# Kernel optimization log

Hardware: AMD Instinct MI355X
Metric: run time of the kernel (lower is better)

## Reference

```python
import jax, jax.numpy as jnp
import numpy as np

S, V, E, H = 4096, 10000, 128, 256
NE, TK, NH, HD, FF, NL = 4, 2, 4, 64, 2048, 2
EPS = 1e-5
SCALE = 1.0 / np.sqrt(HD).astype(np.float32)


def setup_inputs() -> dict:
    key = jax.random.key(0)
    ks = iter(jax.random.split(key, 64))
    n = lambda shape: jax.random.normal(next(ks), shape, jnp.float32) * 0.02
    inp = {"x": jax.random.randint(next(ks), (S,), 0, V)}
    inp["emb"] = n((V, E))
    for i, din in enumerate([E, H, H]):
        inp[f"moe{i}_gw"] = n((NE, din))
        inp[f"moe{i}_gb"] = jnp.zeros((NE,), jnp.float32)
        inp[f"moe{i}_ew"] = n((NE, H, din))
        inp[f"moe{i}_eb"] = jnp.zeros((NE, H), jnp.float32)
    inp["attn_in_w"] = n((NL, 3 * H, H)); inp["attn_in_b"] = jnp.zeros((NL, 3 * H), jnp.float32)
    inp["attn_out_w"] = n((NL, H, H));    inp["attn_out_b"] = jnp.zeros((NL, H), jnp.float32)
    inp["ln1_g"] = jnp.ones((NL, H), jnp.float32); inp["ln1_b"] = jnp.zeros((NL, H), jnp.float32)
    inp["ln2_g"] = jnp.ones((NL, H), jnp.float32); inp["ln2_b"] = jnp.zeros((NL, H), jnp.float32)
    inp["ff1_w"] = n((NL, FF, H)); inp["ff1_b"] = jnp.zeros((NL, FF), jnp.float32)
    inp["ff2_w"] = n((NL, H, FF)); inp["ff2_b"] = jnp.zeros((NL, H), jnp.float32)
    inp["fc_w"] = n((H, H)); inp["fc_b"] = jnp.zeros((H,), jnp.float32)
    inp["out_w"] = n((V, H)); inp["out_b"] = jnp.zeros((V,), jnp.float32)
    return inp


def _ln(x, g, b):
    m = x.mean(-1, keepdims=True)
    v = ((x - m) ** 2).mean(-1, keepdims=True)
    return (x - m) * jax.lax.rsqrt(v + EPS) * g + b


def _moe(x, gw, gb, ew, eb):
    # x: [S, din]. Faithful quirk: experts are the top-k of TOKEN 0's gates,
    # applied to every token, weighted by each token's own top-k gate scores.
    scores = jax.nn.softmax(x @ gw.T + gb, axis=-1)            # [S, NE]
    vals, idx = jax.lax.top_k(scores, TK)                      # [S, TK]
    sel = idx[0]                                               # [TK]
    outs = jnp.einsum('si,khi->skh', x, ew[sel]) + eb[sel][None]  # [S, TK, H]
    return (outs * vals[:, :, None]).sum(axis=1)               # [S, H]


def reference(x, emb,
              moe0_gw, moe0_gb, moe0_ew, moe0_eb,
              moe1_gw, moe1_gb, moe1_ew, moe1_eb,
              moe2_gw, moe2_gb, moe2_ew, moe2_eb,
              attn_in_w, attn_in_b, attn_out_w, attn_out_b,
              ln1_g, ln1_b, ln2_g, ln2_b,
              ff1_w, ff1_b, ff2_w, ff2_b,
              fc_w, fc_b, out_w, out_b):
    h = emb[x]                                                 # [S, E]
    for gw, gb, ew, eb in [(moe0_gw, moe0_gb, moe0_ew, moe0_eb),
                           (moe1_gw, moe1_gb, moe1_ew, moe1_eb),
                           (moe2_gw, moe2_gb, moe2_ew, moe2_eb)]:
        h = _moe(h, gw, gb, ew, eb)                            # [S, H]
    for l in range(NL):  # post-norm TransformerEncoderLayer (relu, no dropout at eval)
        qkv = h @ attn_in_w[l].T + attn_in_b[l]                # [S, 3H]
        q, k, v = [t.reshape(S, NH, HD) for t in jnp.split(qkv, 3, axis=-1)]
        att = jax.nn.softmax(jnp.einsum('shd,thd->hst', q, k) * SCALE, axis=-1)
        a = jnp.einsum('hst,thd->shd', att, v).reshape(S, H)
        h = _ln(h + a @ attn_out_w[l].T + attn_out_b[l], ln1_g[l], ln1_b[l])
        ffh = jax.nn.relu(h @ ff1_w[l].T + ff1_b[l]) @ ff2_w[l].T + ff2_b[l]
        h = _ln(h + ffh, ln2_g[l], ln2_b[l])
    h = h @ fc_w.T + fc_b                                      # [S, H]
    logits = h @ out_w.T + out_b                               # [S, V]
    return jax.nn.log_softmax(logits, axis=-1)
```

## Files before the change

### kernel.cpp

```cpp
#include <hip/hip_runtime.h>
#include <math.h>

#define S_ 4096
#define V_ 10000
#define E_ 128
#define H_ 256
#define NE_ 4
#define NH_ 4
#define HD_ 64
#define FF_ 2048
#define NL_ 2
#define EPS_ 1e-5f
#define SCALE_ 0.125f
#define SPLITS_ 4
#define PSTRIDE_ 160

typedef __attribute__((ext_vector_type(8))) short bf16x8;
typedef __attribute__((ext_vector_type(4))) float f32x4;

static __device__ __forceinline__ short f2bf(float f) {
  unsigned u = __builtin_bit_cast(unsigned, f);
  unsigned r = (u + 0x7fffu + ((u >> 16) & 1u)) >> 16;
  return (short)r;
}
static __device__ __forceinline__ float bf2f(short s) {
  unsigned u = ((unsigned)(unsigned short)s) << 16;
  return __builtin_bit_cast(float, u);
}

struct CvtArgs {
  const float* src[9];
  short* dst[9];
  int pfx[10];
};
__global__ __launch_bounds__(256) void k_cvt(CvtArgs a) {
  int b = blockIdx.x, s = 0;
  while (b >= a.pfx[s + 1]) ++s;
  size_t base = (size_t)(b - a.pfx[s]) * 2048 + threadIdx.x * 8;
  const float* sp = a.src[s] + base;
  short* dp = a.dst[s] + base;
  float4 v0 = *(const float4*)sp;
  float4 v1 = *(const float4*)(sp + 4);
  short4 o0, o1;
  o0.x = f2bf(v0.x); o0.y = f2bf(v0.y); o0.z = f2bf(v0.z); o0.w = f2bf(v0.w);
  o1.x = f2bf(v1.x); o1.y = f2bf(v1.y); o1.z = f2bf(v1.z); o1.w = f2bf(v1.w);
  *(short4*)dp = o0;
  *(short4*)(dp + 4) = o1;
}

__global__ __launch_bounds__(256) void k_embed(const int* __restrict__ x,
                                               const float* __restrict__ emb,
                                               short* __restrict__ h) {
  int i4 = (blockIdx.x * 256 + threadIdx.x) * 4;
  int s = i4 >> 7, e = i4 & 127;
  float4 v = *(const float4*)&emb[(size_t)x[s] * E_ + e];
  short4 o;
  o.x = f2bf(v.x); o.y = f2bf(v.y); o.z = f2bf(v.z); o.w = f2bf(v.w);
  *(short4*)&h[i4] = o;
}

__global__ __launch_bounds__(256) void k_gates(const short* __restrict__ X, int din,
                                               const float* __restrict__ gw,
                                               const float* __restrict__ gb,
                                               float* __restrict__ vals,
                                               int* __restrict__ sel) {
  int wave = threadIdx.x >> 6, lane = threadIdx.x & 63;
  int s = blockIdx.x * 4 + wave;
  const short* xs = X + (size_t)s * din;
  float a0 = 0.f, a1 = 0.f, a2 = 0.f, a3 = 0.f;
  for (int i = lane; i < din; i += 64) {
    float xv = bf2f(xs[i]);
    a0 += xv * gw[0 * din + i];
    a1 += xv * gw[1 * din + i];
    a2 += xv * gw[2 * din + i];
    a3 += xv * gw[3 * din + i];
  }
#pragma unroll
  for (int off = 32; off > 0; off >>= 1) {
    a0 += __shfl_xor(a0, off, 64);
    a1 += __shfl_xor(a1, off, 64);
    a2 += __shfl_xor(a2, off, 64);
    a3 += __shfl_xor(a3, off, 64);
  }
  if (lane == 0) {
    float sc[4] = {a0 + gb[0], a1 + gb[1], a2 + gb[2], a3 + gb[3]};
    float mx = fmaxf(fmaxf(sc[0], sc[1]), fmaxf(sc[2], sc[3]));
    float sum = 0.f;
#pragma unroll
    for (int e = 0; e < 4; ++e) { sc[e] = expf(sc[e] - mx); sum += sc[e]; }
    float inv = 1.0f / sum;
#pragma unroll
    for (int e = 0; e < 4; ++e) sc[e] *= inv;
    int i0 = 0; float v0 = sc[0];
#pragma unroll
    for (int e = 1; e < 4; ++e) if (sc[e] > v0) { v0 = sc[e]; i0 = e; }
    float v1 = -1.0f; int i1 = 0;
#pragma unroll
    for (int e = 0; e < 4; ++e) if (e != i0 && sc[e] > v1) { v1 = sc[e]; i1 = e; }
    vals[2 * s + 0] = v0;
    vals[2 * s + 1] = v1;
    if (s == 0) { sel[0] = i0; sel[1] = i1; }
  }
}

template <int ACT>
__global__ __launch_bounds__(256) void k_gemm64(const short* __restrict__ A,
                                                const short* __restrict__ W,
                                                const float* __restrict__ bias,
                                                short* __restrict__ C,
                                                int M, int N, int K) {
  __shared__ short As[64][40];
  __shared__ short Bs[64][40];
  int bm = blockIdx.y * 64, bn = blockIdx.x * 64;
  int tid = threadIdx.x, lane = tid & 63, wv = tid >> 6;
  int quad = lane >> 4, m16 = lane & 15;
  int wr = (wv >> 1) * 32, wc = (wv & 1) * 32;
  int srow = tid >> 2, sc = (tid & 3) * 8;
  const short* Ar = A + (size_t)(bm + srow) * K + sc;
  const short* Wr = W + (size_t)(bn + srow) * K + sc;
  f32x4 acc[2][2];
#pragma unroll
  for (int m = 0; m < 2; ++m)
#pragma unroll
    for (int n = 0; n < 2; ++n) acc[m][n] = (f32x4){0.f, 0.f, 0.f, 0.f};
  for (int k0 = 0; k0 < K; k0 += 32) {
    *(bf16x8*)&As[srow][sc] = *(const bf16x8*)&Ar[k0];
    *(bf16x8*)&Bs[srow][sc] = *(const bf16x8*)&Wr[k0];
    __syncthreads();
    bf16x8 af[2], bf[2];
#pragma unroll
    for (int m = 0; m < 2; ++m) af[m] = *(const bf16x8*)&As[wr + m * 16 + m16][quad * 8];
#pragma unroll
    for (int n = 0; n < 2; ++n) bf[n] = *(const bf16x8*)&Bs[wc + n * 16 + m16][quad * 8];
#pragma unroll
    for (int m = 0; m < 2; ++m)
#pragma unroll
      for (int n = 0; n < 2; ++n)
        acc[m][n] = __builtin_amdgcn_mfma_f32_16x16x32_bf16(af[m], bf[n], acc[m][n], 0, 0, 0);
    __syncthreads();
  }
#pragma unroll
  for (int n = 0; n < 2; ++n) {
    int col = bn + wc + n * 16 + m16;
    float b = bias[col];
#pragma unroll
    for (int m = 0; m < 2; ++m) {
      int row0 = bm + wr + m * 16 + quad * 4;
#pragma unroll
      for (int r = 0; r < 4; ++r) {
        float v = acc[m][n][r] + b;
        if (ACT) v = fmaxf(v, 0.f);
        C[(size_t)(row0 + r) * N + col] = f2bf(v);
      }
    }
  }
}

template <int ACT>
__global__ __launch_bounds__(256) void k_gemm32(const short* __restrict__ A,
                                                const short* __restrict__ W,
                                                const float* __restrict__ bias,
                                                short* __restrict__ C,
                                                int M, int N, int K) {
  __shared__ short As[32][40];
  __shared__ short Bs[64][40];
  int bm = blockIdx.y * 32, bn = blockIdx.x * 64;
  int tid = threadIdx.x, lane = tid & 63, wv = tid >> 6;
  int quad = lane >> 4, m16 = lane & 15;
  int wr = (wv >> 1) * 16, wc = (wv & 1) * 32;
  int srow = tid >> 2, sc = (tid & 3) * 8;
  const short* Ar = A + (size_t)(bm + (srow & 31)) * K + sc;
  const short* Wr = W + (size_t)(bn + srow) * K + sc;
  f32x4 acc[2];
  acc[0] = (f32x4){0.f, 0.f, 0.f, 0.f};
  acc[1] = (f32x4){0.f, 0.f, 0.f, 0.f};
  for (int k0 = 0; k0 < K; k0 += 32) {
    if (tid < 128) *(bf16x8*)&As[srow][sc] = *(const bf16x8*)&Ar[k0];
    *(bf16x8*)&Bs[srow][sc] = *(const bf16x8*)&Wr[k0];
    __syncthreads();
    bf16x8 af = *(const bf16x8*)&As[wr + m16][quad * 8];
    bf16x8 bf0 = *(const bf16x8*)&Bs[wc + m16][quad * 8];
    bf16x8 bf1 = *(const bf16x8*)&Bs[wc + 16 + m16][quad * 8];
    acc[0] = __builtin_amdgcn_mfma_f32_16x16x32_bf16(af, bf0, acc[0], 0, 0, 0);
    acc[1] = __builtin_amdgcn_mfma_f32_16x16x32_bf16(af, bf1, acc[1], 0, 0, 0);
    __syncthreads();
  }
#pragma unroll
  for (int n = 0; n < 2; ++n) {
    int col = bn + wc + n * 16 + m16;
    float b = bias[col];
    int row0 = bm + wr + quad * 4;
#pragma unroll
    for (int r = 0; r < 4; ++r) {
      float v = acc[n][r] + b;
      if (ACT) v = fmaxf(v, 0.f);
      C[(size_t)(row0 + r) * N + col] = f2bf(v);
    }
  }
}

__global__ __launch_bounds__(256) void k_moe(const short* __restrict__ A,
                                             const short* __restrict__ EW,
                                             const float* __restrict__ EB,
                                             const float* __restrict__ vals,
                                             const int* __restrict__ sel,
                                             short* __restrict__ C,
                                             int N, int K) {
  __shared__ short As[32][40];
  __shared__ short B0s[64][40];
  __shared__ short B1s[64][40];
  int e0 = sel[0], e1 = sel[1];
  const short* W0 = EW + (size_t)e0 * N * K;
  const short* W1 = EW + (size_t)e1 * N * K;
  const float* b0 = EB + (size_t)e0 * N;
  const float* b1 = EB + (size_t)e1 * N;
  int bm = blockIdx.y * 32, bn = blockIdx.x * 64;
  int tid = threadIdx.x, lane = tid & 63, wv = tid >> 6;
  int quad = lane >> 4, m16 = lane & 15;
  int wr = (wv >> 1) * 16, wc = (wv & 1) * 32;
  int srow = tid >> 2, sc = (tid & 3) * 8;
  const short* Ar = A + (size_t)(bm + (srow & 31)) * K + sc;
  const short* W0r = W0 + (size_t)(bn + srow) * K + sc;
  const short* W1r = W1 + (size_t)(bn + srow) * K + sc;
  f32x4 a0[2], a1[2];
  a0[0] = a0[1] = (f32x4){0.f, 0.f, 0.f, 0.f};
  a1[0] = a1[1] = (f32x4){0.f, 0.f, 0.f, 0.f};
  for (int k0 = 0; k0 < K; k0 += 32) {
    if (tid < 128) *(bf16x8*)&As[srow][sc] = *(const bf16x8*)&Ar[k0];
    *(bf16x8*)&B0s[srow][sc] = *(const bf16x8*)&W0r[k0];
    *(bf16x8*)&B1s[srow][sc] = *(const bf16x8*)&W1r[k0];
    __syncthreads();
    bf16x8 af = *(const bf16x8*)&As[wr + m16][quad * 8];
#pragma unroll
    for (int n = 0; n < 2; ++n) {
      bf16x8 bf0 = *(const bf16x8*)&B0s[wc + n * 16 + m16][quad * 8];
      bf16x8 bf1 = *(const bf16x8*)&B1s[wc + n * 16 + m16][quad * 8];
      a0[n] = __builtin_amdgcn_mfma_f32_16x16x32_bf16(af, bf0, a0[n], 0, 0, 0);
      a1[n] = __builtin_amdgcn_mfma_f32_16x16x32_bf16(af, bf1, a1[n], 0, 0, 0);
    }
    __syncthreads();
  }
#pragma unroll
  for (int n = 0; n < 2; ++n) {
    int col = bn + wc + n * 16 + m16;
    float bb0 = b0[col], bb1 = b1[col];
    int row0 = bm + wr + quad * 4;
#pragma unroll
    for (int r = 0; r < 4; ++r) {
      int row = row0 + r;
      float v = vals[2 * row] * (a0[n][r] + bb0) + vals[2 * row + 1] * (a1[n][r] + bb1);
      C[(size_t)row * N + col] = f2bf(v);
    }
  }
}

template <int ACT>
__global__ __launch_bounds__(256) void k_gemm128(const short* __restrict__ A,
                                                 const short* __restrict__ W,
                                                 const float* __restrict__ bias,
                                                 short* __restrict__ C,
                                                 int M, int N, int K) {
  __shared__ short As[128][40];
  __shared__ short Bs[128][40];
  int bm = blockIdx.y * 128, bn = blockIdx.x * 128;
  int tid = threadIdx.x, lane = tid & 63, wv = tid >> 6;
  int quad = lane >> 4, m16 = lane & 15;
  int wr = (wv >> 1) * 64, wc = (wv & 1) * 64;
  int srow = tid >> 1, sc = (tid & 1) * 16;
  const short* Ar = A + (size_t)(bm + srow) * K + sc;
  const short* Wr = W + (size_t)(bn + srow) * K + sc;
  f32x4 acc[4][4];
#pragma unroll
  for (int m = 0; m < 4; ++m)
#pragma unroll
    for (int n = 0; n < 4; ++n) acc[m][n] = (f32x4){0.f, 0.f, 0.f, 0.f};
  for (int k0 = 0; k0 < K; k0 += 32) {
    *(bf16x8*)&As[srow][sc] = *(const bf16x8*)&Ar[k0];
    *(bf16x8*)&As[srow][sc + 8] = *(const bf16x8*)&Ar[k0 + 8];
    *(bf16x8*)&Bs[srow][sc] = *(const bf16x8*)&Wr[k0];
    *(bf16x8*)&Bs[srow][sc + 8] = *(const bf16x8*)&Wr[k0 + 8];
    __syncthreads();
    bf16x8 af[4], bf[4];
#pragma unroll
    for (int m = 0; m < 4; ++m) af[m] = *(const bf16x8*)&As[wr + m * 16 + m16][quad * 8];
#pragma unroll
    for (int n = 0; n < 4; ++n) bf[n] = *(const bf16x8*)&Bs[wc + n * 16 + m16][quad * 8];
#pragma unroll
    for (int m = 0; m < 4; ++m)
#pragma unroll
      for (int n = 0; n < 4; ++n)
        acc[m][n] = __builtin_amdgcn_mfma_f32_16x16x32_bf16(af[m], bf[n], acc[m][n], 0, 0, 0);
    __syncthreads();
  }
#pragma unroll
  for (int n = 0; n < 4; ++n) {
    int col = bn + wc + n * 16 + m16;
    float b = bias[col];
#pragma unroll
    for (int m = 0; m < 4; ++m) {
      int row0 = bm + wr + m * 16 + quad * 4;
#pragma unroll
      for (int r = 0; r < 4; ++r) {
        float v = acc[m][n][r] + b;
        if (ACT) v = fmaxf(v, 0.f);
        C[(size_t)(row0 + r) * N + col] = f2bf(v);
      }
    }
  }
}

__global__ __launch_bounds__(256) void k_gsum(const short* __restrict__ A,
                                              const short* __restrict__ W,
                                              const float* __restrict__ bias,
                                              float* __restrict__ psums,
                                              int M, int N, int K) {
  __shared__ short As[128][40];
  __shared__ short Bs[128][40];
  int bm = blockIdx.y * 128, bn = blockIdx.x * 128;
  int tid = threadIdx.x, lane = tid & 63, wv = tid >> 6;
  int quad = lane >> 4, m16 = lane & 15;
  int wr = (wv >> 1) * 64, wc = (wv & 1) * 64;
  int srow = tid >> 1, sc = (tid & 1) * 16;
  const short* Ar = A + (size_t)(bm + srow) * K + sc;
  int br = bn + srow;
  const short* Wr = W + (size_t)(br < N ? br : N - 1) * K + sc;
  f32x4 acc[4][4];
#pragma unroll
  for (int m = 0; m < 4; ++m)
#pragma unroll
    for (int n = 0; n < 4; ++n) acc[m][n] = (f32x4){0.f, 0.f, 0.f, 0.f};
  for (int k0 = 0; k0 < K; k0 += 32) {
    *(bf16x8*)&As[srow][sc] = *(const bf16x8*)&Ar[k0];
    *(bf16x8*)&As[srow][sc + 8] = *(const bf16x8*)&Ar[k0 + 8];
    *(bf16x8*)&Bs[srow][sc] = *(const bf16x8*)&Wr[k0];
    *(bf16x8*)&Bs[srow][sc + 8] = *(const bf16x8*)&Wr[k0 + 8];
    __syncthreads();
    bf16x8 af[4], bf[4];
#pragma unroll
    for (int m = 0; m < 4; ++m) af[m] = *(const bf16x8*)&As[wr + m * 16 + m16][quad * 8];
#pragma unroll
    for (int n = 0; n < 4; ++n) bf[n] = *(const bf16x8*)&Bs[wc + n * 16 + m16][quad * 8];
#pragma unroll
    for (int m = 0; m < 4; ++m)
#pragma unroll
      for (int n = 0; n < 4; ++n)
        acc[m][n] = __builtin_amdgcn_mfma_f32_16x16x32_bf16(af[m], bf[n], acc[m][n], 0, 0, 0);
    __syncthreads();
  }
  float bcol[4];
  int cvalid[4];
#pragma unroll
  for (int n = 0; n < 4; ++n) {
    int col = bn + wc + n * 16 + m16;
    cvalid[n] = (col < N);
    bcol[n] = cvalid[n] ? bias[col] : 0.f;
  }
  int pslot = blockIdx.x * 2 + (wv & 1);
#pragma unroll
  for (int m = 0; m < 4; ++m) {
#pragma unroll
    for (int r = 0; r < 4; ++r) {
      int row = bm + wr + m * 16 + quad * 4 + r;
      float es = 0.f;
#pragma unroll
      for (int n = 0; n < 4; ++n) {
        if (cvalid[n]) {
          float v = acc[m][n][r] + bcol[n];
          es += __expf(v);
        }
      }
#pragma unroll
      for (int mask = 1; mask < 16; mask <<= 1) es += __shfl_xor(es, mask, 16);
      if (m16 == 0) psums[(size_t)row * PSTRIDE_ + pslot] = es;
    }
  }
}

__global__ __launch_bounds__(256) void k_lse(const float* __restrict__ psums,
                                             float* __restrict__ lse, int nslots) {
  int wv = threadIdx.x >> 6, lane = threadIdx.x & 63;
  int s = blockIdx.x * 4 + wv;
  float a = 0.f;
  for (int i = lane; i < nslots; i += 64) a += psums[(size_t)s * PSTRIDE_ + i];
#pragma unroll
  for (int mask = 1; mask < 64; mask <<= 1) a += __shfl_xor(a, mask, 64);
  if (lane == 0) lse[s] = logf(a);
}

__global__ __launch_bounds__(256) void k_gout(const short* __restrict__ A,
                                              const short* __restrict__ W,
                                              const float* __restrict__ bias,
                                              const float* __restrict__ lse,
                                              float* __restrict__ C,
                                              int M, int N, int K) {
  __shared__ short As[128][40];
  __shared__ short Bs[128][40];
  int bm = blockIdx.y * 128, bn = blockIdx.x * 128;
  int tid = threadIdx.x, lane = tid & 63, wv = tid >> 6;
  int quad = lane >> 4, m16 = lane & 15;
  int wr = (wv >> 1) * 64, wc = (wv & 1) * 64;
  int srow = tid >> 1, sc = (tid & 1) * 16;
  const short* Ar = A + (size_t)(bm + srow) * K + sc;
  int br = bn + srow;
  const short* Wr = W + (size_t)(br < N ? br : N - 1) * K + sc;
  f32x4 acc[4][4];
#pragma unroll
  for (int m = 0; m < 4; ++m)
#pragma unroll
    for (int n = 0; n < 4; ++n) acc[m][n] = (f32x4){0.f, 0.f, 0.f, 0.f};
  for (int k0 = 0; k0 < K; k0 += 32) {
    *(bf16x8*)&As[srow][sc] = *(const bf16x8*)&Ar[k0];
    *(bf16x8*)&As[srow][sc + 8] = *(const bf16x8*)&Ar[k0 + 8];
    *(bf16x8*)&Bs[srow][sc] = *(const bf16x8*)&Wr[k0];
    *(bf16x8*)&Bs[srow][sc + 8] = *(const bf16x8*)&Wr[k0 + 8];
    __syncthreads();
    bf16x8 af[4], bf[4];
#pragma unroll
    for (int m = 0; m < 4; ++m) af[m] = *(const bf16x8*)&As[wr + m * 16 + m16][quad * 8];
#pragma unroll
    for (int n = 0; n < 4; ++n) bf[n] = *(const bf16x8*)&Bs[wc + n * 16 + m16][quad * 8];
#pragma unroll
    for (int m = 0; m < 4; ++m)
#pragma unroll
      for (int n = 0; n < 4; ++n)
        acc[m][n] = __builtin_amdgcn_mfma_f32_16x16x32_bf16(af[m], bf[n], acc[m][n], 0, 0, 0);
    __syncthreads();
  }
  float bcol[4];
  int cvalid[4];
#pragma unroll
  for (int n = 0; n < 4; ++n) {
    int col = bn + wc + n * 16 + m16;
    cvalid[n] = (col < N);
    bcol[n] = cvalid[n] ? bias[col] : 0.f;
  }
#pragma unroll
  for (int m = 0; m < 4; ++m) {
#pragma unroll
    for (int r = 0; r < 4; ++r) {
      int row = bm + wr + m * 16 + quad * 4 + r;
      float flse = lse[row];
#pragma unroll
      for (int n = 0; n < 4; ++n) {
        if (cvalid[n]) {
          float v = acc[m][n][r] + bcol[n] - flse;
          C[(size_t)row * N + (bn + wc + n * 16 + m16)] = v;
        }
      }
    }
  }
}

__global__ __launch_bounds__(256) void k_attn(const short* __restrict__ qkv,
                                              float* __restrict__ Opart,
                                              float* __restrict__ Lpart) {
  __shared__ short Ks[64][72];
  __shared__ short Vt[64][72];
  int tid = threadIdx.x, lane = tid & 63, wv = tid >> 6;
  int quad = lane >> 4, m16 = lane & 15;
  int head = blockIdx.y, hd0 = head * HD_;
  int split = blockIdx.z;
  int qbaseA = blockIdx.x * 128 + wv * 16;
  int qbaseB = qbaseA + 64;
  bf16x8 qfA[2], qfB[2];
  {
    const short* qrA = qkv + (size_t)(qbaseA + m16) * (3 * H_) + hd0 + quad * 8;
    qfA[0] = *(const bf16x8*)&qrA[0];
    qfA[1] = *(const bf16x8*)&qrA[32];
    const short* qrB = qkv + (size_t)(qbaseB + m16) * (3 * H_) + hd0 + quad * 8;
    qfB[0] = *(const bf16x8*)&qrB[0];
    qfB[1] = *(const bf16x8*)&qrB[32];
  }
  f32x4 oA[4], oB[4];
#pragma unroll
  for (int dt = 0; dt < 4; ++dt) {
    oA[dt] = (f32x4){0.f, 0.f, 0.f, 0.f};
    oB[dt] = (f32x4){0.f, 0.f, 0.f, 0.f};
  }
  float lA = 0.f, lB = 0.f;

  int kb_end = (split + 1) * (S_ / 64 / SPLITS_);
  for (int kb = split * (S_ / 64 / SPLITS_); kb < kb_end; ++kb) {
    __syncthreads();
    {
      int key = tid >> 2, d0 = (tid & 3) * 16;
      const short* kr = qkv + (size_t)(kb * 64 + key) * (3 * H_) + H_ + hd0 + d0;
      *(bf16x8*)&Ks[key][d0] = *(const bf16x8*)&kr[0];
      *(bf16x8*)&Ks[key][d0 + 8] = *(const bf16x8*)&kr[8];
    }
    {
      int key0 = (tid & 15) * 4, d0 = (tid >> 4) * 4;
      const short* vbase = qkv + (size_t)(kb * 64 + key0) * (3 * H_) + 2 * H_ + hd0 + d0;
      short4 v0 = *(const short4*)&vbase[0];
      short4 v1 = *(const short4*)&vbase[3 * H_];
      short4 v2 = *(const short4*)&vbase[6 * H_];
      short4 v3 = *(const short4*)&vbase[9 * H_];
      short4 t0 = {v0.x, v1.x, v2.x, v3.x};
      short4 t1 = {v0.y, v1.y, v2.y, v3.y};
      short4 t2 = {v0.z, v1.z, v2.z, v3.z};
      short4 t3 = {v0.w, v1.w, v2.w, v3.w};
      *(short4*)&Vt[d0 + 0][key0] = t0;
      *(short4*)&Vt[d0 + 1][key0] = t1;
      *(short4*)&Vt[d0 + 2][key0] = t2;
      *(short4*)&Vt[d0 + 3][key0] = t3;
    }
    __syncthreads();
    f32x4 sA[4], sB[4];
#pragma unroll
    for (int kt = 0; kt < 4; ++kt) {
      bf16x8 ak0 = *(const bf16x8*)&Ks[kt * 16 + m16][quad * 8];
      bf16x8 ak1 = *(const bf16x8*)&Ks[kt * 16 + m16][32 + quad * 8];
      f32x4 zA = (f32x4){0.f, 0.f, 0.f, 0.f};
      zA = __builtin_amdgcn_mfma_f32_16x16x32_bf16(ak0, qfA[0], zA, 0, 0, 0);
      zA = __builtin_amdgcn_mfma_f32_16x16x32_bf16(ak1, qfA[1], zA, 0, 0, 0);
      sA[kt] = zA;
      f32x4 zB = (f32x4){0.f, 0.f, 0.f, 0.f};
      zB = __builtin_amdgcn_mfma_f32_16x16x32_bf16(ak0, qfB[0], zB, 0, 0, 0);
      zB = __builtin_amdgcn_mfma_f32_16x16x32_bf16(ak1, qfB[1], zB, 0, 0, 0);
      sB[kt] = zB;
    }
    unsigned pwA[4][2], pwB[4][2];
    {
      float rsum = 0.f;
#pragma unroll
      for (int kt = 0; kt < 4; ++kt) {
        float p0 = __expf(sA[kt][0] * SCALE_);
        float p1 = __expf(sA[kt][1] * SCALE_);
        float p2 = __expf(sA[kt][2] * SCALE_);
        float p3 = __expf(sA[kt][3] * SCALE_);
        rsum += (p0 + p1) + (p2 + p3);
        asm("v_cvt_pk_bf16_f32 %0, %1, %2" : "=v"(pwA[kt][0]) : "v"(p0), "v"(p1));
        asm("v_cvt_pk_bf16_f32 %0, %1, %2" : "=v"(pwA[kt][1]) : "v"(p2), "v"(p3));
      }
      unsigned ua = __builtin_bit_cast(unsigned, rsum), ub = ua;
      asm volatile("v_permlane16_swap_b32 %0, %1" : "+v"(ua), "+v"(ub));
      float s01 = __builtin_bit_cast(float, ua) + __builtin_bit_cast(float, ub);
      unsigned uc = __builtin_bit_cast(unsigned, s01), ud = uc;
      asm volatile("v_permlane32_swap_b32 %0, %1" : "+v"(uc), "+v"(ud));
      lA += __builtin_bit_cast(float, uc) + __builtin_bit_cast(float, ud);
    }
    {
      float rsum = 0.f;
#pragma unroll
      for (int kt = 0; kt < 4; ++kt) {
        float p0 = __expf(sB[kt][0] * SCALE_);
        float p1 = __expf(sB[kt][1] * SCALE_);
        float p2 = __expf(sB[kt][2] * SCALE_);
        float p3 = __expf(sB[kt][3] * SCALE_);
        rsum += (p0 + p1) + (p2 + p3);
        asm("v_cvt_pk_bf16_f32 %0, %1, %2" : "=v"(pwB[kt][0]) : "v"(p0), "v"(p1));
        asm("v_cvt_pk_bf16_f32 %0, %1, %2" : "=v"(pwB[kt][1]) : "v"(p2), "v"(p3));
      }
      unsigned ua = __builtin_bit_cast(unsigned, rsum), ub = ua;
      asm volatile("v_permlane16_swap_b32 %0, %1" : "+v"(ua), "+v"(ub));
      float s01 = __builtin_bit_cast(float, ua) + __builtin_bit_cast(float, ub);
      unsigned uc = __builtin_bit_cast(unsigned, s01), ud = uc;
      asm volatile("v_permlane32_swap_b32 %0, %1" : "+v"(uc), "+v"(ud));
      lB += __builtin_bit_cast(float, uc) + __builtin_bit_cast(float, ud);
    }
#pragma unroll
    for (int c = 0; c < 2; ++c) {
      unsigned a0 = pwA[2 * c][0], b0 = pwA[2 * c + 1][0];
      asm volatile("v_permlane32_swap_b32 %0, %1" : "+v"(a0), "+v"(b0));
      asm volatile("v_permlane16_swap_b32 %0, %1" : "+v"(a0), "+v"(b0));
      unsigned a1 = pwA[2 * c][1], b1 = pwA[2 * c + 1][1];
      asm volatile("v_permlane32_swap_b32 %0, %1" : "+v"(a1), "+v"(b1));
      asm volatile("v_permlane16_swap_b32 %0, %1" : "+v"(a1), "+v"(b1));
      union { unsigned u[4]; bf16x8 v; } puA;
      puA.u[0] = a0; puA.u[1] = a1; puA.u[2] = b0; puA.u[3] = b1;
      bf16x8 paA = puA.v;
      unsigned c0 = pwB[2 * c][0], d0w = pwB[2 * c + 1][0];
      asm volatile("v_permlane32_swap_b32 %0, %1" : "+v"(c0), "+v"(d0w));
      asm volatile("v_permlane16_swap_b32 %0, %1" : "+v"(c0), "+v"(d0w));
      unsigned c1 = pwB[2 * c][1], d1w = pwB[2 * c + 1][1];
      asm volatile("v_permlane32_swap_b32 %0, %1" : "+v"(c1), "+v"(d1w));
      asm volatile("v_permlane16_swap_b32 %0, %1" : "+v"(c1), "+v"(d1w));
      union { unsigned u[4]; bf16x8 v; } puB;
      puB.u[0] = c0; puB.u[1] = c1; puB.u[2] = d0w; puB.u[3] = d1w;
      bf16x8 paB = puB.v;
#pragma unroll
      for (int dt = 0; dt < 4; ++dt) {
        bf16x8 bv = *(const bf16x8*)&Vt[dt * 16 + m16][c * 32 + quad * 8];
        oA[dt] = __builtin_amdgcn_mfma_f32_16x16x32_bf16(paA, bv, oA[dt], 0, 0, 0);
        oB[dt] = __builtin_amdgcn_mfma_f32_16x16x32_bf16(paB, bv, oB[dt], 0, 0, 0);
      }
    }
  }
  float* Op = Opart + ((size_t)(split * NH_ + head) * S_) * 64;
#pragma unroll
  for (int dt = 0; dt < 4; ++dt) {
#pragma unroll
    for (int r = 0; r < 4; ++r) {
      int rowA = qbaseA + quad * 4 + r;
      Op[(size_t)rowA * 64 + dt * 16 + m16] = oA[dt][r];
      int rowB = qbaseB + quad * 4 + r;
      Op[(size_t)rowB * 64 + dt * 16 + m16] = oB[dt][r];
    }
  }
  if (quad == 0) {
    float* Lp = Lpart + (size_t)(split * NH_ + head) * S_;
    Lp[qbaseA + m16] = lA;
    Lp[qbaseB + m16] = lB;
  }
}

__global__ __launch_bounds__(256) void k_att_combine(const float* __restrict__ Opart,
                                                     const float* __restrict__ Lpart,
                                                     short* __restrict__ abuf) {
  int idx = blockIdx.x * 256 + threadIdx.x;
  int s = idx >> 8, hd = idx & 255;
  int head = hd >> 6, d = hd & 63;
  float num = 0.f, den = 0.f;
#pragma unroll
  for (int sp = 0; sp < SPLITS_; ++sp) {
    num += Opart[((size_t)(sp * NH_ + head) * S_ + s) * 64 + d];
    den += Lpart[(size_t)(sp * NH_ + head) * S_ + s];
  }
  abuf[idx] = f2bf(num / den);
}

__global__ __launch_bounds__(256) void k_add_ln(short* __restrict__ h,
                                                const short* __restrict__ t_,
                                                const float* __restrict__ g,
                                                const float* __restrict__ b) {
  int wv = threadIdx.x >> 6, lane = threadIdx.x & 63;
  int s = blockIdx.x * 4 + wv;
  size_t off = (size_t)s * H_ + lane * 4;
  short4 hv = *(const short4*)&h[off];
  short4 tv = *(const short4*)&t_[off];
  float x[4] = {bf2f(hv.x) + bf2f(tv.x), bf2f(hv.y) + bf2f(tv.y),
                bf2f(hv.z) + bf2f(tv.z), bf2f(hv.w) + bf2f(tv.w)};
  float sum = x[0] + x[1] + x[2] + x[3];
#pragma unroll
  for (int mask = 1; mask < 64; mask <<= 1) sum += __shfl_xor(sum, mask, 64);
  float mean = sum * (1.0f / H_);
  float d[4], vs = 0.f;
#pragma unroll
  for (int i = 0; i < 4; ++i) { d[i] = x[i] - mean; vs += d[i] * d[i]; }
#pragma unroll
  for (int mask = 1; mask < 64; mask <<= 1) vs += __shfl_xor(vs, mask, 64);
  float inv = rsqrtf(vs * (1.0f / H_) + EPS_);
  float4 gv = *(const float4*)&g[lane * 4];
  float4 bv = *(const float4*)&b[lane * 4];
  short4 ov;
  ov.x = f2bf(d[0] * inv * gv.x + bv.x);
  ov.y = f2bf(d[1] * inv * gv.y + bv.y);
  ov.z = f2bf(d[2] * inv * gv.z + bv.z);
  ov.w = f2bf(d[3] * inv * gv.w + bv.w);
  *(short4*)&h[off] = ov;
}

extern "C" void kernel_launch(void* const* d_in, const int* in_sizes, int n_in,
                              void* d_out, int out_size, void* d_ws, size_t ws_size,
                              hipStream_t stream) {
  const int* x = (const int*)d_in[0];
  const float* emb = (const float*)d_in[1];
  const float* moe_gw[3] = {(const float*)d_in[2], (const float*)d_in[6], (const float*)d_in[10]};
  const float* moe_gb[3] = {(const float*)d_in[3], (const float*)d_in[7], (const float*)d_in[11]};
  const float* moe_eb[3] = {(const float*)d_in[5], (const float*)d_in[9], (const float*)d_in[13]};
  const float* attn_in_b = (const float*)d_in[15];
  const float* attn_out_b = (const float*)d_in[17];
  const float* ln1_g = (const float*)d_in[18];
  const float* ln1_b = (const float*)d_in[19];
  const float* ln2_g = (const float*)d_in[20];
  const float* ln2_b = (const float*)d_in[21];
  const float* ff1_b = (const float*)d_in[23];
  const float* ff2_b = (const float*)d_in[25];
  const float* fc_b = (const float*)d_in[27];
  const float* out_b = (const float*)d_in[29];
  float* out = (float*)d_out;

  short* wsS = (short*)d_ws;
  size_t off = 0;
  auto alloc = [&](size_t n) { short* p = wsS + off; off += n; return p; };
  short* ewb0 = alloc(131072);
  short* ewb1 = alloc(262144);
  short* ewb2 = alloc(262144);
  short* aiwb = alloc(393216);
  short* aowb = alloc(131072);
  short* f1wb = alloc(1048576);
  short* f2wb = alloc(1048576);
  short* fcwb = alloc(65536);
  short* owb  = alloc(2560000);
  short* hb_e = alloc((size_t)S_ * E_);
  short* hb_a = alloc((size_t)S_ * H_);
  short* hb_b = alloc((size_t)S_ * H_);
  short* qkvb = alloc((size_t)S_ * 3 * H_);
  short* abufb = alloc((size_t)S_ * H_);
  short* tmpb = alloc((size_t)S_ * H_);
  short* ffhb = alloc((size_t)S_ * FF_);
  float* vals = (float*)(wsS + off); off += 2 * (size_t)S_ * 2;
  int* sel = (int*)(wsS + off);
  float* Opart = (float*)ffhb;
  float* Lpart = (float*)tmpb;
  float* psums = (float*)f1wb;
  float* lse = psums + (size_t)S_ * PSTRIDE_;

  const short* moe_ewb[3] = {ewb0, ewb1, ewb2};

  CvtArgs ca;
  ca.src[0] = (const float*)d_in[4];  ca.dst[0] = ewb0;
  ca.src[1] = (const float*)d_in[8];  ca.dst[1] = ewb1;
  ca.src[2] = (const float*)d_in[12]; ca.dst[2] = ewb2;
  ca.src[3] = (const float*)d_in[14]; ca.dst[3] = aiwb;
  ca.src[4] = (const float*)d_in[16]; ca.dst[4] = aowb;
  ca.src[5] = (const float*)d_in[22]; ca.dst[5] = f1wb;
  ca.src[6] = (const float*)d_in[24]; ca.dst[6] = f2wb;
  ca.src[7] = (const float*)d_in[26]; ca.dst[7] = fcwb;
  ca.src[8] = (const float*)d_in[28]; ca.dst[8] = owb;
  int sizes[9] = {131072, 262144, 262144, 393216, 131072, 1048576, 1048576, 65536, 2560000};
  ca.pfx[0] = 0;
  for (int i = 0; i < 9; ++i) ca.pfx[i + 1] = ca.pfx[i] + sizes[i] / 2048;
  k_cvt<<<dim3(ca.pfx[9]), dim3(256), 0, stream>>>(ca);

  k_embed<<<dim3(S_ * E_ / 1024), dim3(256), 0, stream>>>(x, emb, hb_e);

  const short* moe_in[3] = {hb_e, hb_a, hb_b};
  short* moe_out[3] = {hb_a, hb_b, hb_a};
  int moe_k[3] = {E_, H_, H_};
  for (int i = 0; i < 3; ++i) {
    k_gates<<<dim3(S_ / 4), dim3(256), 0, stream>>>(moe_in[i], moe_k[i], moe_gw[i], moe_gb[i], vals, sel);
    k_moe<<<dim3(H_ / 64, S_ / 32), dim3(256), 0, stream>>>(moe_in[i], moe_ewb[i], moe_eb[i],
                                                            vals, sel, moe_out[i], H_, moe_k[i]);
  }

  for (int l = 0; l < NL_; ++l) {
    k_gemm64<0><<<dim3(3 * H_ / 64, S_ / 64), dim3(256), 0, stream>>>(
        hb_a, aiwb + (size_t)l * 3 * H_ * H_, attn_in_b + (size_t)l * 3 * H_, qkvb, S_, 3 * H_, H_);
    k_attn<<<dim3(S_ / 128, NH_, SPLITS_), dim3(256), 0, stream>>>(qkvb, Opart, Lpart);
    k_att_combine<<<dim3(S_ * H_ / 256), dim3(256), 0, stream>>>(Opart, Lpart, abufb);
    k_gemm32<0><<<dim3(H_ / 64, S_ / 32), dim3(256), 0, stream>>>(
        abufb, aowb + (size_t)l * H_ * H_, attn_out_b + (size_t)l * H_, tmpb, S_, H_, H_);
    k_add_ln<<<dim3(S_ / 4), dim3(256), 0, stream>>>(hb_a, tmpb, ln1_g + l * H_, ln1_b + l * H_);
    k_gemm128<1><<<dim3(FF_ / 128, S_ / 128), dim3(256), 0, stream>>>(
        hb_a, f1wb + (size_t)l * FF_ * H_, ff1_b + (size_t)l * FF_, ffhb, S_, FF_, H_);
    k_gemm32<0><<<dim3(H_ / 64, S_ / 32), dim3(256), 0, stream>>>(
        ffhb, f2wb + (size_t)l * H_ * FF_, ff2_b + (size_t)l * H_, tmpb, S_, H_, FF_);
    k_add_ln<<<dim3(S_ / 4), dim3(256), 0, stream>>>(hb_a, tmpb, ln2_g + l * H_, ln2_b + l * H_);
  }

  k_gemm32<0><<<dim3(H_ / 64, S_ / 32), dim3(256), 0, stream>>>(hb_a, fcwb, fc_b, tmpb, S_, H_, H_);
  int nxb = (V_ + 127) / 128;
  k_gsum<<<dim3(nxb, S_ / 128), dim3(256), 0, stream>>>(tmpb, owb, out_b, psums, S_, V_, H_);
  k_lse<<<dim3(S_ / 4), dim3(256), 0, stream>>>(psums, lse, nxb * 2);
  k_gout<<<dim3(nxb, S_ / 128), dim3(256), 0, stream>>>(tmpb, owb, out_b, lse, out, S_, V_, H_);
}
```

Measured before the change: 597.7 us.

## Fuse attention split-combine into out-proj GEMM, embed into cvt, widen FF2 K-tile

```diff
diff --git a/kernel.cpp b/kernel.cpp
--- a/kernel.cpp
+++ b/kernel.cpp
@@ -33,8 +33,24 @@
   short* dst[9];
   int pfx[10];
 };
-__global__ __launch_bounds__(256) void k_cvt(CvtArgs a) {
-  int b = blockIdx.x, s = 0;
+__global__ __launch_bounds__(256) void k_cvt(CvtArgs a, const int* __restrict__ x,
+                                             const float* __restrict__ emb,
+                                             short* __restrict__ h) {
+  int b = blockIdx.x;
+  if (b >= a.pfx[9]) {
+    int i8 = (b - a.pfx[9]) * 2048 + threadIdx.x * 8;
+    int s = i8 >> 7, e = i8 & 127;
+    const float* sp = &emb[(size_t)x[s] * E_ + e];
+    float4 v0 = *(const float4*)sp;
+    float4 v1 = *(const float4*)(sp + 4);
+    short4 o0, o1;
+    o0.x = f2bf(v0.x); o0.y = f2bf(v0.y); o0.z = f2bf(v0.z); o0.w = f2bf(v0.w);
+    o1.x = f2bf(v1.x); o1.y = f2bf(v1.y); o1.z = f2bf(v1.z); o1.w = f2bf(v1.w);
+    *(short4*)&h[i8] = o0;
+    *(short4*)&h[i8 + 4] = o1;
+    return;
+  }
+  int s = 0;
   while (b >= a.pfx[s + 1]) ++s;
   size_t base = (size_t)(b - a.pfx[s]) * 2048 + threadIdx.x * 8;
   const float* sp = a.src[s] + base;
@@ -46,17 +62,6 @@
   o1.x = f2bf(v1.x); o1.y = f2bf(v1.y); o1.z = f2bf(v1.z); o1.w = f2bf(v1.w);
   *(short4*)dp = o0;
   *(short4*)(dp + 4) = o1;
-}
-
-__global__ __launch_bounds__(256) void k_embed(const int* __restrict__ x,
-                                               const float* __restrict__ emb,
-                                               short* __restrict__ h) {
-  int i4 = (blockIdx.x * 256 + threadIdx.x) * 4;
-  int s = i4 >> 7, e = i4 & 127;
-  float4 v = *(const float4*)&emb[(size_t)x[s] * E_ + e];
-  short4 o;
-  o.x = f2bf(v.x); o.y = f2bf(v.y); o.z = f2bf(v.z); o.w = f2bf(v.w);
-  *(short4*)&h[i4] = o;
 }
 
 __global__ __launch_bounds__(256) void k_gates(const short* __restrict__ X, int din,
@@ -195,6 +200,125 @@
       float v = acc[n][r] + b;
       if (ACT) v = fmaxf(v, 0.f);
       C[(size_t)(row0 + r) * N + col] = f2bf(v);
+    }
+  }
+}
+
+__global__ __launch_bounds__(256) void k_proj(const float* __restrict__ Opart,
+                                              const float* __restrict__ Lpart,
+                                              const short* __restrict__ W,
+                                              const float* __restrict__ bias,
+                                              short* __restrict__ C) {
+  __shared__ short As[32][40];
+  __shared__ short Bs[64][40];
+  int bm = blockIdx.y * 32, bn = blockIdx.x * 64;
+  int tid = threadIdx.x, lane = tid & 63, wv = tid >> 6;
+  int quad = lane >> 4, m16 = lane & 15;
+  int wr = (wv >> 1) * 16, wc = (wv & 1) * 32;
+  int srow = tid >> 2, sc = (tid & 3) * 8;
+  int rowA = bm + (srow & 31);
+  const short* Wr = W + (size_t)(bn + srow) * H_ + sc;
+  float invden[NH_];
+  if (tid < 128) {
+#pragma unroll
+    for (int hh = 0; hh < NH_; ++hh) {
+      float dsum = 0.f;
+#pragma unroll
+      for (int sp = 0; sp < SPLITS_; ++sp)
+        dsum += Lpart[(size_t)(sp * NH_ + hh) * S_ + rowA];
+      invden[hh] = 1.0f / dsum;
+    }
+  }
+  f32x4 acc[2];
+  acc[0] = (f32x4){0.f, 0.f, 0.f, 0.f};
+  acc[1] = (f32x4){0.f, 0.f, 0.f, 0.f};
+#pragma unroll
+  for (int k0 = 0; k0 < H_; k0 += 32) {
+    if (tid < 128) {
+      const int head = k0 >> 6;
+      int dd = (k0 & 63) + sc;
+      float n0 = 0.f, n1 = 0.f, n2 = 0.f, n3 = 0.f, n4 = 0.f, n5 = 0.f, n6 = 0.f, n7 = 0.f;
+#pragma unroll
+      for (int sp = 0; sp < SPLITS_; ++sp) {
+        const float* op = &Opart[((size_t)(sp * NH_ + head) * S_ + rowA) * 64 + dd];
+        float4 u0 = *(const float4*)op;
+        float4 u1 = *(const float4*)(op + 4);
+        n0 += u0.x; n1 += u0.y; n2 += u0.z; n3 += u0.w;
+        n4 += u1.x; n5 += u1.y; n6 += u1.z; n7 += u1.w;
+      }
+      float iv = invden[head];
+      union { short s[8]; bf16x8 v; } o;
+      o.s[0] = f2bf(n0 * iv); o.s[1] = f2bf(n1 * iv);
+      o.s[2] = f2bf(n2 * iv); o.s[3] = f2bf(n3 * iv);
+      o.s[4] = f2bf(n4 * iv); o.s[5] = f2bf(n5 * iv);
+      o.s[6] = f2bf(n6 * iv); o.s[7] = f2bf(n7 * iv);
+      *(bf16x8*)&As[srow][sc] = o.v;
+    }
+    *(bf16x8*)&Bs[srow][sc] = *(const bf16x8*)&Wr[k0];
+    __syncthreads();
+    bf16x8 af = *(const bf16x8*)&As[wr + m16][quad * 8];
+    bf16x8 bf0 = *(const bf16x8*)&Bs[wc + m16][quad * 8];
+    bf16x8 bf1 = *(const bf16x8*)&Bs[wc + 16 + m16][quad * 8];
+    acc[0] = __builtin_amdgcn_mfma_f32_16x16x32_bf16(af, bf0, acc[0], 0, 0, 0);
+    acc[1] = __builtin_amdgcn_mfma_f32_16x16x32_bf16(af, bf1, acc[1], 0, 0, 0);
+    __syncthreads();
+  }
+#pragma unroll
+  for (int n = 0; n < 2; ++n) {
+    int col = bn + wc + n * 16 + m16;
+    float b = bias[col];
+    int row0 = bm + wr + quad * 4;
+#pragma unroll
+    for (int r = 0; r < 4; ++r) {
+      float v = acc[n][r] + b;
+      C[(size_t)(row0 + r) * H_ + col] = f2bf(v);
+    }
+  }
+}
+
+__global__ __launch_bounds__(256) void k_ff2(const short* __restrict__ A,
+                                             const short* __restrict__ W,
+                                             const float* __restrict__ bias,
+                                             short* __restrict__ C) {
+  __shared__ short As[32][72];
+  __shared__ short Bs[64][72];
+  int bm = blockIdx.y * 32, bn = blockIdx.x * 64;
+  int tid = threadIdx.x, lane = tid & 63, wv = tid >> 6;
+  int quad = lane >> 4, m16 = lane & 15;
+  int wr = (wv >> 1) * 16, wc = (wv & 1) * 32;
+  int arow = tid >> 3, ac = (tid & 7) * 8;
+  int brow = tid >> 2, bc = (tid & 3) * 16;
+  const short* Ar = A + (size_t)(bm + arow) * FF_ + ac;
+  const short* Wr = W + (size_t)(bn + brow) * FF_ + bc;
+  f32x4 acc[2];
+  acc[0] = (f32x4){0.f, 0.f, 0.f, 0.f};
+  acc[1] = (f32x4){0.f, 0.f, 0.f, 0.f};
+  for (int k0 = 0; k0 < FF_; k0 += 64) {
+    *(bf16x8*)&As[arow][ac] = *(const bf16x8*)&Ar[k0];
+    *(bf16x8*)&Bs[brow][bc] = *(const bf16x8*)&Wr[k0];
+    *(bf16x8*)&Bs[brow][bc + 8] = *(const bf16x8*)&Wr[k0 + 8];
+    __syncthreads();
+    bf16x8 af0 = *(const bf16x8*)&As[wr + m16][quad * 8];
+    bf16x8 af1 = *(const bf16x8*)&As[wr + m16][32 + quad * 8];
+    bf16x8 b00 = *(const bf16x8*)&Bs[wc + m16][quad * 8];
+    bf16x8 b01 = *(const bf16x8*)&Bs[wc + m16][32 + quad * 8];
+    bf16x8 b10 = *(const bf16x8*)&Bs[wc + 16 + m16][quad * 8];
+    bf16x8 b11 = *(const bf16x8*)&Bs[wc + 16 + m16][32 + quad * 8];
+    acc[0] = __builtin_amdgcn_mfma_f32_16x16x32_bf16(af0, b00, acc[0], 0, 0, 0);
+    acc[0] = __builtin_amdgcn_mfma_f32_16x16x32_bf16(af1, b01, acc[0], 0, 0, 0);
+    acc[1] = __builtin_amdgcn_mfma_f32_16x16x32_bf16(af0, b10, acc[1], 0, 0, 0);
+    acc[1] = __builtin_amdgcn_mfma_f32_16x16x32_bf16(af1, b11, acc[1], 0, 0, 0);
+    __syncthreads();
+  }
+#pragma unroll
+  for (int n = 0; n < 2; ++n) {
+    int col = bn + wc + n * 16 + m16;
+    float b = bias[col];
+    int row0 = bm + wr + quad * 4;
+#pragma unroll
+    for (int r = 0; r < 4; ++r) {
+      float v = acc[n][r] + b;
+      C[(size_t)(row0 + r) * H_ + col] = f2bf(v);
     }
   }
 }
@@ -604,21 +728,6 @@
   }
 }
 
-__global__ __launch_bounds__(256) void k_att_combine(const float* __restrict__ Opart,
-                                                     const float* __restrict__ Lpart,
-                                                     short* __restrict__ abuf) {
-  int idx = blockIdx.x * 256 + threadIdx.x;
-  int s = idx >> 8, hd = idx & 255;
-  int head = hd >> 6, d = hd & 63;
-  float num = 0.f, den = 0.f;
-#pragma unroll
-  for (int sp = 0; sp < SPLITS_; ++sp) {
-    num += Opart[((size_t)(sp * NH_ + head) * S_ + s) * 64 + d];
-    den += Lpart[(size_t)(sp * NH_ + head) * S_ + s];
-  }
-  abuf[idx] = f2bf(num / den);
-}
-
 __global__ __launch_bounds__(256) void k_add_ln(short* __restrict__ h,
                                                 const short* __restrict__ t_,
                                                 const float* __restrict__ g,
@@ -711,9 +820,7 @@
   int sizes[9] = {131072, 262144, 262144, 393216, 131072, 1048576, 1048576, 65536, 2560000};
   ca.pfx[0] = 0;
   for (int i = 0; i < 9; ++i) ca.pfx[i + 1] = ca.pfx[i] + sizes[i] / 2048;
-  k_cvt<<<dim3(ca.pfx[9]), dim3(256), 0, stream>>>(ca);
-
-  k_embed<<<dim3(S_ * E_ / 1024), dim3(256), 0, stream>>>(x, emb, hb_e);
+  k_cvt<<<dim3(ca.pfx[9] + S_ * E_ / 2048), dim3(256), 0, stream>>>(ca, x, emb, hb_e);
 
   const short* moe_in[3] = {hb_e, hb_a, hb_b};
   short* moe_out[3] = {hb_a, hb_b, hb_a};
@@ -728,14 +835,13 @@
     k_gemm64<0><<<dim3(3 * H_ / 64, S_ / 64), dim3(256), 0, stream>>>(
         hb_a, aiwb + (size_t)l * 3 * H_ * H_, attn_in_b + (size_t)l * 3 * H_, qkvb, S_, 3 * H_, H_);
     k_attn<<<dim3(S_ / 128, NH_, SPLITS_), dim3(256), 0, stream>>>(qkvb, Opart, Lpart);
-    k_att_combine<<<dim3(S_ * H_ / 256), dim3(256), 0, stream>>>(Opart, Lpart, abufb);
-    k_gemm32<0><<<dim3(H_ / 64, S_ / 32), dim3(256), 0, stream>>>(
-        abufb, aowb + (size_t)l * H_ * H_, attn_out_b + (size_t)l * H_, tmpb, S_, H_, H_);
+    k_proj<<<dim3(H_ / 64, S_ / 32), dim3(256), 0, stream>>>(
+        Opart, Lpart, aowb + (size_t)l * H_ * H_, attn_out_b + (size_t)l * H_, tmpb);
     k_add_ln<<<dim3(S_ / 4), dim3(256), 0, stream>>>(hb_a, tmpb, ln1_g + l * H_, ln1_b + l * H_);
     k_gemm128<1><<<dim3(FF_ / 128, S_ / 128), dim3(256), 0, stream>>>(
         hb_a, f1wb + (size_t)l * FF_ * H_, ff1_b + (size_t)l * FF_, ffhb, S_, FF_, H_);
-    k_gemm32<0><<<dim3(H_ / 64, S_ / 32), dim3(256), 0, stream>>>(
-        ffhb, f2wb + (size_t)l * H_ * FF_, ff2_b + (size_t)l * H_, tmpb, S_, H_, FF_);
+    k_ff2<<<dim3(H_ / 64, S_ / 32), dim3(256), 0, stream>>>(
+        ffhb, f2wb + (size_t)l * H_ * FF_, ff2_b + (size_t)l * H_, tmpb);
     k_add_ln<<<dim3(S_ / 4), dim3(256), 0, stream>>>(hb_a, tmpb, ln2_g + l * H_, ln2_b + l * H_);
   }
 
```

Result: faster. 582.6 us (-2.5%).
